# Kernel tuning notes

Measured on AMD Instinct MI355X. Metric: run time of the kernel, lower is better.

## Reference

```python
import jax, jax.numpy as jnp
import numpy as np

SMOOTH_AMP = 0.15   # smoothing_factor in _apply_emd_constrained_smoothing
SMOOTH_PH = 0.10    # smoothing_factor in _apply_spatial_smoothing
PERIODS = (0.25, 0.5, 1.0, 2.0)
TWO_PI = 2.0 * np.pi


def setup_inputs() -> dict:
    N, T, K, P = 50000, 1000, 8, 4
    key = jax.random.key(0)
    ks = jax.random.split(key, 9)
    time_vector = jax.random.uniform(ks[0], (T,), jnp.float32) * 10.0  # years
    constant_offset = jax.random.normal(ks[1], (N,), jnp.float32) * 5.0
    linear_trend = jax.random.normal(ks[2], (N,), jnp.float32) * 2.0  # ps00 rates
    seasonal_amplitudes = jax.random.uniform(ks[3], (N, P), jnp.float32) * 10.0  # init ~5.0
    seasonal_phases = jax.random.uniform(ks[4], (N, P), jnp.float32) * TWO_PI
    w = jax.random.uniform(ks[5], (N, K), jnp.float32)
    neighbor_weights = w / (jnp.sum(w, axis=1, keepdims=True) + 1e-6)  # row-normalized as in kNN graph
    bounds_min = jax.random.uniform(ks[6], (P, N), jnp.float32) * 5.0
    bounds_max = bounds_min + 5.0 + jax.random.uniform(ks[7], (P, N), jnp.float32) * 40.0
    neighbor_indices = jax.random.randint(ks[8], (N, K), 0, N, jnp.int32)
    return {
        'time_vector': time_vector,
        'constant_offset': constant_offset,
        'linear_trend': linear_trend,
        'seasonal_amplitudes': seasonal_amplitudes,
        'seasonal_phases': seasonal_phases,
        'neighbor_weights': neighbor_weights,
        'bounds_min': bounds_min,
        'bounds_max': bounds_max,
        'neighbor_indices': neighbor_indices,
    }


def reference(time_vector, constant_offset, linear_trend, seasonal_amplitudes,
              seasonal_phases, neighbor_weights, bounds_min, bounds_max,
              neighbor_indices):
    t = time_vector[None, :]                                   # [1,T]
    signals = constant_offset[:, None] + linear_trend[:, None] * t  # [N,T]
    for i, period in enumerate(PERIODS):
        amp = seasonal_amplitudes[:, i]                        # [N]
        ph = seasonal_phases[:, i]                             # [N]
        # EMD-constrained amplitude smoothing: gather neighbors, weighted avg, mix, clamp
        nbr_avg = jnp.sum(amp[neighbor_indices] * neighbor_weights, axis=-1)  # [N]
        s_amp = jnp.clip((1.0 - SMOOTH_AMP) * amp + SMOOTH_AMP * nbr_avg,
                         bounds_min[i], bounds_max[i])
        # circular (complex) phase smoothing
        cr, ci = jnp.cos(ph), jnp.sin(ph)
        ar = jnp.sum(cr[neighbor_indices] * neighbor_weights, axis=-1)
        ai = jnp.sum(ci[neighbor_indices] * neighbor_weights, axis=-1)
        mr = (1.0 - SMOOTH_PH) * cr + SMOOTH_PH * ar
        mi = (1.0 - SMOOTH_PH) * ci + SMOOTH_PH * ai
        s_ph = jnp.arctan2(mi, mr)
        freq = 1.0 / period
        signals = signals + s_amp[:, None] * jnp.sin(TWO_PI * freq * t + s_ph[:, None])
    return signals
```

## Files before the change

### kernel.cpp

```cpp
#include <hip/hip_runtime.h>
#include <math.h>

#define INV_TWO_PI_F 0.15915494309189535f

__device__ __forceinline__ void sincos_rev(float rev, float* s, float* c) {
    float r = rev - floorf(rev);
    *s = __builtin_amdgcn_sinf(r);
    *c = __builtin_amdgcn_cosf(r);
}

template <int ROWS, int U, int KT>
__global__ __launch_bounds__(256, 4) void k_all(
        const float* __restrict__ tv,   const float* __restrict__ co,
        const float* __restrict__ lt,   const float* __restrict__ amp,
        const float* __restrict__ ph,   const float* __restrict__ w,
        const float* __restrict__ bmin, const float* __restrict__ bmax,
        const int* __restrict__ nbr,
        float* __restrict__ out, int N, int T, int Krt) {
    const int tid   = threadIdx.x;
    const int nq    = (T + 3) >> 2;
    const int qi    = blockIdx.y * 256 + tid;
    const int t0    = qi * 4;
    const bool act  = (qi < nq);
    const int nbase = blockIdx.x * ROWS;
    const int K     = KT ? KT : Krt;

    __shared__ float cf[ROWS][12];

    if (tid < ROWS * 4) {
        const int r = tid >> 2, i = tid & 3;
        const int n = nbase + r;
        if (n < N) {
            float na = 0.f, ar = 0.f, ai = 0.f;
#pragma unroll
            for (int k = 0; k < K; ++k) {
                const float wk = w[(size_t)n * K + k];
                const int   m  = nbr[(size_t)n * K + k];
                const float am = amp[(size_t)m * 4 + i];
                const float pm = ph[(size_t)m * 4 + i];
                float s, c;
                sincos_rev(pm * INV_TWO_PI_F, &s, &c);
                na = fmaf(am, wk, na);
                ar = fmaf(c, wk, ar);
                ai = fmaf(s, wk, ai);
            }
            const float a0 = amp[(size_t)n * 4 + i];
            const float p0 = ph[(size_t)n * 4 + i];
            float s_amp = fmaf(0.15f, na, 0.85f * a0);
            s_amp = fminf(fmaxf(s_amp, bmin[(size_t)i * N + n]),
                          bmax[(size_t)i * N + n]);
            float ci, cr;
            sincos_rev(p0 * INV_TWO_PI_F, &ci, &cr);
            const float mr  = fmaf(0.1f, ar, 0.9f * cr);
            const float mi  = fmaf(0.1f, ai, 0.9f * ci);
            const float inv = rsqrtf(fmaf(mr, mr, mi * mi));
            cf[r][2 * i]     = s_amp * mr * inv;
            cf[r][2 * i + 1] = s_amp * mi * inv;
            if (i == 0) {
                cf[r][8]  = co[n];
                cf[r][9]  = lt[n];
                cf[r][10] = 0.f;
                cf[r][11] = 0.f;
            }
        }
    }

    const float freqs[4] = {4.0f, 2.0f, 1.0f, 0.5f};
    float tvq[4], sn[4][4], cs[4][4];
    if (act) {
#pragma unroll
        for (int q = 0; q < 4; ++q) {
            int t = t0 + q; if (t > T - 1) t = T - 1;
            tvq[q] = tv[t];
#pragma unroll
            for (int i = 0; i < 4; ++i)
                sincos_rev(freqs[i] * tvq[q], &sn[q][i], &cs[q][i]);
        }
    }
    __syncthreads();

    if (act) {
        float* dst = out + (size_t)nbase * T + t0;
#pragma unroll 1
        for (int rb = 0; rb < ROWS; rb += U) {
            float v[U][4];
#pragma unroll
            for (int u = 0; u < U; ++u) {
                const int r = rb + u;
                const float4 PQ0 = *(const float4*)&cf[r][0];
                const float4 PQ1 = *(const float4*)&cf[r][4];
                const float4 CB  = *(const float4*)&cf[r][8];
#pragma unroll
                for (int q = 0; q < 4; ++q) {
                    float x = fmaf(CB.y, tvq[q], CB.x);
                    x = fmaf(PQ0.x, sn[q][0], x);
                    x = fmaf(PQ0.y, cs[q][0], x);
                    x = fmaf(PQ0.z, sn[q][1], x);
                    x = fmaf(PQ0.w, cs[q][1], x);
                    x = fmaf(PQ1.x, sn[q][2], x);
                    x = fmaf(PQ1.y, cs[q][2], x);
                    x = fmaf(PQ1.z, sn[q][3], x);
                    x = fmaf(PQ1.w, cs[q][3], x);
                    v[u][q] = x;
                }
            }
            if (t0 + 3 < T) {
#pragma unroll
                for (int u = 0; u < U; ++u) {
                    const int n = nbase + rb + u;
                    if (n >= N) break;
                    float4 o; o.x = v[u][0]; o.y = v[u][1]; o.z = v[u][2]; o.w = v[u][3];
                    *(float4*)(dst + (size_t)(rb + u) * T) = o;
                }
            } else {
#pragma unroll
                for (int u = 0; u < U; ++u) {
                    const int n = nbase + rb + u;
                    if (n >= N) break;
#pragma unroll
                    for (int q = 0; q < 4; ++q)
                        if (t0 + q < T) *(dst + (size_t)(rb + u) * T + q) = v[u][q];
                }
            }
        }
    }
}

extern "C" void kernel_launch(void* const* d_in, const int* in_sizes, int n_in,
                              void* d_out, int out_size, void* d_ws, size_t ws_size,
                              hipStream_t stream) {
    const float* tv   = (const float*)d_in[0];
    const float* co   = (const float*)d_in[1];
    const float* lt   = (const float*)d_in[2];
    const float* amp  = (const float*)d_in[3];
    const float* ph   = (const float*)d_in[4];
    const float* w    = (const float*)d_in[5];
    const float* bmin = (const float*)d_in[6];
    const float* bmax = (const float*)d_in[7];
    const int*   nbr  = (const int*)d_in[8];

    const int T = in_sizes[0];
    const int N = in_sizes[1];
    const int K = in_sizes[5] / N;

    float* out = (float*)d_out;

    constexpr int ROWS = 50;
    constexpr int U    = 10;
    const int nq = (T + 3) / 4;
    dim3 grid((N + ROWS - 1) / ROWS, (nq + 255) / 256);
    if (K == 8) {
        k_all<ROWS, U, 8><<<grid, 256, 0, stream>>>(tv, co, lt, amp, ph, w, bmin,
                                                    bmax, nbr, out, N, T, K);
    } else {
        k_all<ROWS, U, 0><<<grid, 256, 0, stream>>>(tv, co, lt, amp, ph, w, bmin,
                                                    bmax, nbr, out, N, T, K);
    }
}
```

Measured before the change: 40.47 us.

## Split coefficient smoothing into separate kernel writing per-row phasor coefficients to workspace

```diff
diff --git a/kernel.cpp b/kernel.cpp
--- a/kernel.cpp
+++ b/kernel.cpp
@@ -9,118 +9,126 @@
     *c = __builtin_amdgcn_cosf(r);
 }
 
-template <int ROWS, int U, int KT>
-__global__ __launch_bounds__(256, 4) void k_all(
-        const float* __restrict__ tv,   const float* __restrict__ co,
-        const float* __restrict__ lt,   const float* __restrict__ amp,
-        const float* __restrict__ ph,   const float* __restrict__ w,
+template <int KT>
+__global__ __launch_bounds__(256) void k_coef(
+        const float* __restrict__ amp,  const float* __restrict__ ph,
+        const float* __restrict__ w,    const int* __restrict__ nbr,
         const float* __restrict__ bmin, const float* __restrict__ bmax,
-        const int* __restrict__ nbr,
-        float* __restrict__ out, int N, int T, int Krt) {
+        float* __restrict__ pq, int N, int Krt) {
+    const int n = blockIdx.x * blockDim.x + threadIdx.x;
+    if (n >= N) return;
+    const int K = KT ? KT : Krt;
+
+    float na[4] = {0.f, 0.f, 0.f, 0.f};
+    float ar[4] = {0.f, 0.f, 0.f, 0.f};
+    float ai[4] = {0.f, 0.f, 0.f, 0.f};
+#pragma unroll
+    for (int k = 0; k < K; ++k) {
+        const float wk = w[(size_t)n * K + k];
+        const int   m  = nbr[(size_t)n * K + k];
+        const float4 am = *(const float4*)(amp + (size_t)m * 4);
+        const float4 pm = *(const float4*)(ph + (size_t)m * 4);
+        const float amv[4] = {am.x, am.y, am.z, am.w};
+        const float pmv[4] = {pm.x, pm.y, pm.z, pm.w};
+#pragma unroll
+        for (int i = 0; i < 4; ++i) {
+            float s, c;
+            sincos_rev(pmv[i] * INV_TWO_PI_F, &s, &c);
+            na[i] = fmaf(amv[i], wk, na[i]);
+            ar[i] = fmaf(c, wk, ar[i]);
+            ai[i] = fmaf(s, wk, ai[i]);
+        }
+    }
+    const float4 a0 = *(const float4*)(amp + (size_t)n * 4);
+    const float4 p0 = *(const float4*)(ph + (size_t)n * 4);
+    const float av[4] = {a0.x, a0.y, a0.z, a0.w};
+    const float pv[4] = {p0.x, p0.y, p0.z, p0.w};
+    float o[8];
+#pragma unroll
+    for (int i = 0; i < 4; ++i) {
+        float s_amp = fmaf(0.15f, na[i], 0.85f * av[i]);
+        s_amp = fminf(fmaxf(s_amp, bmin[(size_t)i * N + n]),
+                      bmax[(size_t)i * N + n]);
+        float ci, cr;
+        sincos_rev(pv[i] * INV_TWO_PI_F, &ci, &cr);
+        const float mr  = fmaf(0.1f, ar[i], 0.9f * cr);
+        const float mi  = fmaf(0.1f, ai[i], 0.9f * ci);
+        const float inv = rsqrtf(fmaf(mr, mr, mi * mi));
+        o[2 * i]     = s_amp * mr * inv;
+        o[2 * i + 1] = s_amp * mi * inv;
+    }
+    float4 o0; o0.x = o[0]; o0.y = o[1]; o0.z = o[2]; o0.w = o[3];
+    float4 o1; o1.x = o[4]; o1.y = o[5]; o1.z = o[6]; o1.w = o[7];
+    *(float4*)(pq + (size_t)n * 8)     = o0;
+    *(float4*)(pq + (size_t)n * 8 + 4) = o1;
+}
+
+template <int ROWS, int U>
+__global__ __launch_bounds__(256, 4) void k_sweep(
+        const float* __restrict__ tv, const float* __restrict__ co,
+        const float* __restrict__ lt, const float* __restrict__ pq,
+        float* __restrict__ out, int N, int T) {
     const int tid   = threadIdx.x;
     const int nq    = (T + 3) >> 2;
     const int qi    = blockIdx.y * 256 + tid;
     const int t0    = qi * 4;
     const bool act  = (qi < nq);
     const int nbase = blockIdx.x * ROWS;
-    const int K     = KT ? KT : Krt;
-
-    __shared__ float cf[ROWS][12];
-
-    if (tid < ROWS * 4) {
-        const int r = tid >> 2, i = tid & 3;
-        const int n = nbase + r;
-        if (n < N) {
-            float na = 0.f, ar = 0.f, ai = 0.f;
-#pragma unroll
-            for (int k = 0; k < K; ++k) {
-                const float wk = w[(size_t)n * K + k];
-                const int   m  = nbr[(size_t)n * K + k];
-                const float am = amp[(size_t)m * 4 + i];
-                const float pm = ph[(size_t)m * 4 + i];
-                float s, c;
-                sincos_rev(pm * INV_TWO_PI_F, &s, &c);
-                na = fmaf(am, wk, na);
-                ar = fmaf(c, wk, ar);
-                ai = fmaf(s, wk, ai);
-            }
-            const float a0 = amp[(size_t)n * 4 + i];
-            const float p0 = ph[(size_t)n * 4 + i];
-            float s_amp = fmaf(0.15f, na, 0.85f * a0);
-            s_amp = fminf(fmaxf(s_amp, bmin[(size_t)i * N + n]),
-                          bmax[(size_t)i * N + n]);
-            float ci, cr;
-            sincos_rev(p0 * INV_TWO_PI_F, &ci, &cr);
-            const float mr  = fmaf(0.1f, ar, 0.9f * cr);
-            const float mi  = fmaf(0.1f, ai, 0.9f * ci);
-            const float inv = rsqrtf(fmaf(mr, mr, mi * mi));
-            cf[r][2 * i]     = s_amp * mr * inv;
-            cf[r][2 * i + 1] = s_amp * mi * inv;
-            if (i == 0) {
-                cf[r][8]  = co[n];
-                cf[r][9]  = lt[n];
-                cf[r][10] = 0.f;
-                cf[r][11] = 0.f;
-            }
-        }
-    }
 
     const float freqs[4] = {4.0f, 2.0f, 1.0f, 0.5f};
     float tvq[4], sn[4][4], cs[4][4];
-    if (act) {
 #pragma unroll
-        for (int q = 0; q < 4; ++q) {
-            int t = t0 + q; if (t > T - 1) t = T - 1;
-            tvq[q] = tv[t];
+    for (int q = 0; q < 4; ++q) {
+        int t = t0 + q; if (t > T - 1) t = T - 1;
+        tvq[q] = tv[t];
 #pragma unroll
-            for (int i = 0; i < 4; ++i)
-                sincos_rev(freqs[i] * tvq[q], &sn[q][i], &cs[q][i]);
+        for (int i = 0; i < 4; ++i)
+            sincos_rev(freqs[i] * tvq[q], &sn[q][i], &cs[q][i]);
+    }
+
+    if (!act) return;
+
+    float* dst = out + (size_t)nbase * T + t0;
+#pragma unroll 1
+    for (int rb = 0; rb < ROWS; rb += U) {
+        float v[U][4];
+#pragma unroll
+        for (int u = 0; u < U; ++u) {
+            const int n = nbase + rb + u;
+            const float4 PQ0 = *(const float4*)(pq + (size_t)n * 8);
+            const float4 PQ1 = *(const float4*)(pq + (size_t)n * 8 + 4);
+            const float  c0  = co[n];
+            const float  b   = lt[n];
+#pragma unroll
+            for (int q = 0; q < 4; ++q) {
+                float x = fmaf(b, tvq[q], c0);
+                x = fmaf(PQ0.x, sn[q][0], x);
+                x = fmaf(PQ0.y, cs[q][0], x);
+                x = fmaf(PQ0.z, sn[q][1], x);
+                x = fmaf(PQ0.w, cs[q][1], x);
+                x = fmaf(PQ1.x, sn[q][2], x);
+                x = fmaf(PQ1.y, cs[q][2], x);
+                x = fmaf(PQ1.z, sn[q][3], x);
+                x = fmaf(PQ1.w, cs[q][3], x);
+                v[u][q] = x;
+            }
         }
-    }
-    __syncthreads();
-
-    if (act) {
-        float* dst = out + (size_t)nbase * T + t0;
-#pragma unroll 1
-        for (int rb = 0; rb < ROWS; rb += U) {
-            float v[U][4];
+        if (t0 + 3 < T) {
 #pragma unroll
             for (int u = 0; u < U; ++u) {
-                const int r = rb + u;
-                const float4 PQ0 = *(const float4*)&cf[r][0];
-                const float4 PQ1 = *(const float4*)&cf[r][4];
-                const float4 CB  = *(const float4*)&cf[r][8];
+                const int n = nbase + rb + u;
+                if (n >= N) break;
+                float4 o; o.x = v[u][0]; o.y = v[u][1]; o.z = v[u][2]; o.w = v[u][3];
+                *(float4*)(dst + (size_t)(rb + u) * T) = o;
+            }
+        } else {
 #pragma unroll
-                for (int q = 0; q < 4; ++q) {
-                    float x = fmaf(CB.y, tvq[q], CB.x);
-                    x = fmaf(PQ0.x, sn[q][0], x);
-                    x = fmaf(PQ0.y, cs[q][0], x);
-                    x = fmaf(PQ0.z, sn[q][1], x);
-                    x = fmaf(PQ0.w, cs[q][1], x);
-                    x = fmaf(PQ1.x, sn[q][2], x);
-                    x = fmaf(PQ1.y, cs[q][2], x);
-                    x = fmaf(PQ1.z, sn[q][3], x);
-                    x = fmaf(PQ1.w, cs[q][3], x);
-                    v[u][q] = x;
-                }
-            }
-            if (t0 + 3 < T) {
+            for (int u = 0; u < U; ++u) {
+                const int n = nbase + rb + u;
+                if (n >= N) break;
 #pragma unroll
-                for (int u = 0; u < U; ++u) {
-                    const int n = nbase + rb + u;
-                    if (n >= N) break;
-                    float4 o; o.x = v[u][0]; o.y = v[u][1]; o.z = v[u][2]; o.w = v[u][3];
-                    *(float4*)(dst + (size_t)(rb + u) * T) = o;
-                }
-            } else {
-#pragma unroll
-                for (int u = 0; u < U; ++u) {
-                    const int n = nbase + rb + u;
-                    if (n >= N) break;
-#pragma unroll
-                    for (int q = 0; q < 4; ++q)
-                        if (t0 + q < T) *(dst + (size_t)(rb + u) * T + q) = v[u][q];
-                }
+                for (int q = 0; q < 4; ++q)
+                    if (t0 + q < T) *(dst + (size_t)(rb + u) * T + q) = v[u][q];
             }
         }
     }
@@ -143,17 +151,20 @@
     const int N = in_sizes[1];
     const int K = in_sizes[5] / N;
 
+    float* pq  = (float*)d_ws;
     float* out = (float*)d_out;
+
+    if (K == 8) {
+        k_coef<8><<<(N + 255) / 256, 256, 0, stream>>>(amp, ph, w, nbr, bmin,
+                                                       bmax, pq, N, K);
+    } else {
+        k_coef<0><<<(N + 255) / 256, 256, 0, stream>>>(amp, ph, w, nbr, bmin,
+                                                       bmax, pq, N, K);
+    }
 
     constexpr int ROWS = 50;
     constexpr int U    = 10;
     const int nq = (T + 3) / 4;
     dim3 grid((N + ROWS - 1) / ROWS, (nq + 255) / 256);
-    if (K == 8) {
-        k_all<ROWS, U, 8><<<grid, 256, 0, stream>>>(tv, co, lt, amp, ph, w, bmin,
-                                                    bmax, nbr, out, N, T, K);
-    } else {
-        k_all<ROWS, U, 0><<<grid, 256, 0, stream>>>(tv, co, lt, amp, ph, w, bmin,
-                                                    bmax, nbr, out, N, T, K);
-    }
+    k_sweep<ROWS, U><<<grid, 256, 0, stream>>>(tv, co, lt, pq, out, N, T);
 }
```

Result: slower. 47.72 us (+17.9%).
